# Performance work log

Hardware: AMD Instinct MI355X
Metric: run time of the kernel (lower is better)

Reference implementation:

```python
import jax, jax.numpy as jnp
import numpy as np

B, S, H, D = 2, 2048, 16, 128  # batch, seq, n_head, head_dim; n_embd = H*D
N_EMBD = H * D

def setup_inputs() -> dict:
    key = jax.random.key(0)
    kq, kk, kv = jax.random.split(key, 3)
    q = jax.random.normal(kq, (B, S, H, D), dtype=jnp.float32)
    k = jax.random.normal(kk, (B, S, H, D), dtype=jnp.float32)
    v = jax.random.normal(kv, (B, S, H, D), dtype=jnp.float32)
    return {"q": q, "k": k, "v": v}

def reference(q, k, v):
    # [B,S,H,D] -> [B,H,S,D]
    qh = jnp.transpose(q, (0, 2, 1, 3))
    kh = jnp.transpose(k, (0, 2, 1, 3))
    vh = jnp.transpose(v, (0, 2, 1, 3))
    # scores scaled by head_dim (NOT sqrt), matching the original module
    att = jnp.einsum('bhqd,bhkd->bhqk', qh, kh) / D
    att = jax.nn.softmax(att, axis=-1)
    y = jnp.einsum('bhqk,bhkd->bhqd', att, vh)
    # [B,H,S,D] -> [B,S,H,D] -> [B*S, n_embd]
    y = jnp.transpose(y, (0, 2, 1, 3)).reshape(B * S, N_EMBD)
    return y
```

## Files before the change

kernel.cpp:

```cpp
#include <hip/hip_runtime.h>


#define SEQ   2048
#define NHEAD 16
#define DH    128
#define NB    2
#define BQ    128
#define BK    64
#define NTHR  256
#define KSTR  136
#define VSTR  72
#define NKV   (SEQ / BK)
#define NELEM (NB * SEQ * NHEAD * DH)
#define KTILE (BK * KSTR)
#define VTILE (DH * VSTR)

typedef __attribute__((ext_vector_type(8)))  short bf16x8;
typedef __attribute__((ext_vector_type(16))) float f32x16;
typedef __attribute__((ext_vector_type(4)))  unsigned int u32x4;

__device__ __forceinline__ unsigned short f2bf(float x) {
    unsigned int u = __builtin_bit_cast(unsigned int, x);
    u += 0x7fffu + ((u >> 16) & 1u);
    return (unsigned short)(u >> 16);
}

__device__ __forceinline__ unsigned int bfr(float x) {
    unsigned int u = __builtin_bit_cast(unsigned int, x);
    return (u + 0x8000u) & 0xffff0000u;
}

__device__ __forceinline__ void pl32(unsigned int& a, unsigned int& b) {
    asm("v_permlane32_swap_b32 %0, %1" : "+v"(a), "+v"(b));
}

__global__ __launch_bounds__(256) void cvt_bf16(
    const float* __restrict__ q, const float* __restrict__ k,
    const float* __restrict__ v, unsigned short* __restrict__ dst)
{
    const int y = blockIdx.y;
    const float* s = (y == 0) ? q : (y == 1) ? k : v;
    unsigned short* d = dst + (size_t)y * NELEM;
    const int i = blockIdx.x * 256 + threadIdx.x;
    const float4 x = ((const float4*)s)[i];
    ushort4 o;
    o.x = f2bf(x.x); o.y = f2bf(x.y); o.z = f2bf(x.z); o.w = f2bf(x.w);
    ((ushort4*)d)[i] = o;
}

__global__ __launch_bounds__(NTHR, 2) void attn_fwd(
    const unsigned short* __restrict__ Qb,
    const unsigned short* __restrict__ Kb,
    const unsigned short* __restrict__ Vb,
    float* __restrict__ O)
{
    __shared__ unsigned short Kl[2][KTILE];
    __shared__ unsigned short Vl[2][VTILE];

    const int tid  = threadIdx.x;
    const int wave = tid >> 6;
    const int lane = tid & 63;
    const int hx   = lane >> 5;
    const int l32  = lane & 31;

    const int b  = blockIdx.y >> 4;
    const int h  = blockIdx.y & 15;
    const int q0 = blockIdx.x * BQ;

    const size_t rs = (size_t)NHEAD * DH;
    const unsigned short* qb = Qb + (size_t)b * SEQ * rs + (size_t)h * DH;
    const unsigned short* kb = Kb + (size_t)b * SEQ * rs + (size_t)h * DH;
    const unsigned short* vb = Vb + (size_t)b * SEQ * rs + (size_t)h * DH;

    bf16x8 qf[8];
    {
        const unsigned short* qp = qb + (size_t)(q0 + wave * 32 + l32) * rs + hx * 8;
        #pragma unroll
        for (int c = 0; c < 8; ++c)
            qf[c] = *(const bf16x8*)(qp + c * 16);
    }

    int kgo[4], kls[4];
    #pragma unroll
    for (int p = 0; p < 4; ++p) {
        const int cidx = (wave * 4 + p) * 64 + lane;
        const int key  = cidx >> 4;
        const int cc   = cidx & 15;
        kgo[p] = key * (int)rs + cc * 8;
        kls[p] = key * KSTR + cc * 8;
    }
    const int kp  = tid & 31;
    const int dcv = tid >> 5;

    f32x16 o4[4];
    #pragma unroll
    for (int t = 0; t < 4; ++t)
        #pragma unroll
        for (int r = 0; r < 16; ++r) o4[t][r] = 0.f;
    float lsum = 0.f;
    const float c1 = 1.44269504088896340736f / 128.0f;

    bf16x8 kr[4], vr[4];

    {
        #pragma unroll
        for (int p = 0; p < 4; ++p) kr[p] = *(const bf16x8*)(kb + kgo[p]);
        #pragma unroll
        for (int p = 0; p < 2; ++p) {
            const unsigned short* src = vb + (size_t)(2 * kp) * rs + (dcv + p * 8) * 8;
            vr[p * 2]     = *(const bf16x8*)src;
            vr[p * 2 + 1] = *(const bf16x8*)(src + rs);
        }
        #pragma unroll
        for (int p = 0; p < 4; ++p) *(bf16x8*)&Kl[0][kls[p]] = kr[p];
        unsigned int* vw = (unsigned int*)&Vl[0][0];
        #pragma unroll
        for (int p = 0; p < 2; ++p)
            #pragma unroll
            for (int j = 0; j < 8; ++j) {
                const unsigned int pr = ((unsigned int)(unsigned short)vr[p * 2][j])
                                      | (((unsigned int)(unsigned short)vr[p * 2 + 1][j]) << 16);
                vw[((dcv + p * 8) * 8 + j) * (VSTR / 2) + kp] = pr;
            }
    }
    __syncthreads();

    for (int kv = 0; kv < NKV; ++kv) {
        const int cur = kv & 1;
        const int k0n = ((kv + 1) & (NKV - 1)) * BK;

        #pragma unroll
        for (int p = 0; p < 4; ++p) kr[p] = *(const bf16x8*)(kb + (size_t)k0n * rs + kgo[p]);
        #pragma unroll
        for (int p = 0; p < 2; ++p) {
            const unsigned short* src = vb + (size_t)(k0n + 2 * kp) * rs + (dcv + p * 8) * 8;
            vr[p * 2]     = *(const bf16x8*)src;
            vr[p * 2 + 1] = *(const bf16x8*)(src + rs);
        }

        const unsigned short* Kc = &Kl[cur][0];
        const unsigned short* Vc = &Vl[cur][0];

        #pragma unroll
        for (int kt = 0; kt < 2; ++kt) {
            f32x16 s;
            #pragma unroll
            for (int r = 0; r < 16; ++r) s[r] = 0.f;
            #pragma unroll
            for (int c = 0; c < 8; ++c) {
                bf16x8 kf = *(const bf16x8*)&Kc[(kt * 32 + l32) * KSTR + c * 16 + hx * 8];
                s = __builtin_amdgcn_mfma_f32_32x32x16_bf16(kf, qf[c], s, 0, 0, 0);
            }

            unsigned int w[4][2];
            #pragma unroll
            for (int g = 0; g < 4; ++g) {
                const unsigned int u0 = bfr(__builtin_amdgcn_exp2f(s[g * 4 + 0] * c1));
                const unsigned int u1 = bfr(__builtin_amdgcn_exp2f(s[g * 4 + 1] * c1));
                const unsigned int u2 = bfr(__builtin_amdgcn_exp2f(s[g * 4 + 2] * c1));
                const unsigned int u3 = bfr(__builtin_amdgcn_exp2f(s[g * 4 + 3] * c1));
                lsum += (__builtin_bit_cast(float, u0) + __builtin_bit_cast(float, u1))
                      + (__builtin_bit_cast(float, u2) + __builtin_bit_cast(float, u3));
                w[g][0] = u1 | (u0 >> 16);
                w[g][1] = u3 | (u2 >> 16);
            }

            #pragma unroll
            for (int ks = 0; ks < 2; ++ks) {
                pl32(w[2 * ks][0], w[2 * ks + 1][0]);
                pl32(w[2 * ks][1], w[2 * ks + 1][1]);
            }
            bf16x8 pf[2];
            #pragma unroll
            for (int ks = 0; ks < 2; ++ks) {
                u32x4 t;
                t.x = w[2 * ks][0];
                t.y = w[2 * ks][1];
                t.z = w[2 * ks + 1][0];
                t.w = w[2 * ks + 1][1];
                pf[ks] = __builtin_bit_cast(bf16x8, t);
            }

            #pragma unroll
            for (int ks = 0; ks < 2; ++ks)
                #pragma unroll
                for (int dt = 0; dt < 4; ++dt) {
                    bf16x8 vf = *(const bf16x8*)&Vc[(dt * 32 + l32) * VSTR
                                                    + kt * 32 + ks * 16 + hx * 8];
                    o4[dt] = __builtin_amdgcn_mfma_f32_32x32x16_bf16(pf[ks], vf, o4[dt], 0, 0, 0);
                }
        }

        const int nxt = cur ^ 1;
        #pragma unroll
        for (int p = 0; p < 4; ++p) *(bf16x8*)&Kl[nxt][kls[p]] = kr[p];
        {
            unsigned int* vw = (unsigned int*)&Vl[nxt][0];
            #pragma unroll
            for (int p = 0; p < 2; ++p)
                #pragma unroll
                for (int j = 0; j < 8; ++j) {
                    const unsigned int pr = ((unsigned int)(unsigned short)vr[p * 2][j])
                                          | (((unsigned int)(unsigned short)vr[p * 2 + 1][j]) << 16);
                    vw[((dcv + p * 8) * 8 + j) * (VSTR / 2) + kp] = pr;
                }
        }
        __syncthreads();
    }

    lsum += __shfl_xor(lsum, 32, 64);
    const float inv = 1.0f / lsum;
    float iv[16];
    #pragma unroll
    for (int r = 0; r < 16; ++r)
        iv[r] = __shfl(inv, (r & 3) + 8 * (r >> 2) + 4 * hx, 64);

    #pragma unroll
    for (int dt = 0; dt < 4; ++dt) {
        #pragma unroll
        for (int r = 0; r < 16; ++r) {
            const int ql = (r & 3) + 8 * (r >> 2) + 4 * hx;
            const int qg = q0 + wave * 32 + ql;
            O[(size_t)(b * SEQ + qg) * rs + (size_t)h * DH + dt * 32 + l32] = o4[dt][r] * iv[r];
        }
    }
}

extern "C" void kernel_launch(void* const* d_in, const int* in_sizes, int n_in,
                              void* d_out, int out_size, void* d_ws, size_t ws_size,
                              hipStream_t stream) {
    const float* q = (const float*)d_in[0];
    const float* k = (const float*)d_in[1];
    const float* v = (const float*)d_in[2];
    float* o = (float*)d_out;
    unsigned short* wsb = (unsigned short*)d_ws;

    cvt_bf16<<<dim3(NELEM / 1024, 3), 256, 0, stream>>>(q, k, v, wsb);
    attn_fwd<<<dim3(SEQ / BQ, NB * NHEAD), dim3(NTHR), 0, stream>>>(
        wsb, wsb + NELEM, wsb + 2 * (size_t)NELEM, o);
}
```

Measured before the change: 214.1 us.

## Double query tile and threads per block to share K/V staging

```diff
diff --git a/kernel.cpp b/kernel.cpp
--- a/kernel.cpp
+++ b/kernel.cpp
@@ -5,9 +5,9 @@
 #define NHEAD 16
 #define DH    128
 #define NB    2
-#define BQ    128
+#define BQ    256
 #define BK    64
-#define NTHR  256
+#define NTHR  512
 #define KSTR  136
 #define VSTR  72
 #define NKV   (SEQ / BK)
@@ -80,10 +80,10 @@
             qf[c] = *(const bf16x8*)(qp + c * 16);
     }
 
-    int kgo[4], kls[4];
-    #pragma unroll
-    for (int p = 0; p < 4; ++p) {
-        const int cidx = (wave * 4 + p) * 64 + lane;
+    int kgo[2], kls[2];
+    #pragma unroll
+    for (int p = 0; p < 2; ++p) {
+        const int cidx = p * NTHR + tid;
         const int key  = cidx >> 4;
         const int cc   = cidx & 15;
         kgo[p] = key * (int)rs + cc * 8;
@@ -100,28 +100,25 @@
     float lsum = 0.f;
     const float c1 = 1.44269504088896340736f / 128.0f;
 
-    bf16x8 kr[4], vr[4];
+    bf16x8 kr[2], vr[2];
 
     {
         #pragma unroll
-        for (int p = 0; p < 4; ++p) kr[p] = *(const bf16x8*)(kb + kgo[p]);
-        #pragma unroll
-        for (int p = 0; p < 2; ++p) {
-            const unsigned short* src = vb + (size_t)(2 * kp) * rs + (dcv + p * 8) * 8;
-            vr[p * 2]     = *(const bf16x8*)src;
-            vr[p * 2 + 1] = *(const bf16x8*)(src + rs);
-        }
-        #pragma unroll
-        for (int p = 0; p < 4; ++p) *(bf16x8*)&Kl[0][kls[p]] = kr[p];
+        for (int p = 0; p < 2; ++p) kr[p] = *(const bf16x8*)(kb + kgo[p]);
+        {
+            const unsigned short* src = vb + (size_t)(2 * kp) * rs + dcv * 8;
+            vr[0] = *(const bf16x8*)src;
+            vr[1] = *(const bf16x8*)(src + rs);
+        }
+        #pragma unroll
+        for (int p = 0; p < 2; ++p) *(bf16x8*)&Kl[0][kls[p]] = kr[p];
         unsigned int* vw = (unsigned int*)&Vl[0][0];
         #pragma unroll
-        for (int p = 0; p < 2; ++p)
-            #pragma unroll
-            for (int j = 0; j < 8; ++j) {
-                const unsigned int pr = ((unsigned int)(unsigned short)vr[p * 2][j])
-                                      | (((unsigned int)(unsigned short)vr[p * 2 + 1][j]) << 16);
-                vw[((dcv + p * 8) * 8 + j) * (VSTR / 2) + kp] = pr;
-            }
+        for (int j = 0; j < 8; ++j) {
+            const unsigned int pr = ((unsigned int)(unsigned short)vr[0][j])
+                                  | (((unsigned int)(unsigned short)vr[1][j]) << 16);
+            vw[(dcv * 8 + j) * (VSTR / 2) + kp] = pr;
+        }
     }
     __syncthreads();
 
@@ -130,12 +127,11 @@
         const int k0n = ((kv + 1) & (NKV - 1)) * BK;
 
         #pragma unroll
-        for (int p = 0; p < 4; ++p) kr[p] = *(const bf16x8*)(kb + (size_t)k0n * rs + kgo[p]);
-        #pragma unroll
-        for (int p = 0; p < 2; ++p) {
-            const unsigned short* src = vb + (size_t)(k0n + 2 * kp) * rs + (dcv + p * 8) * 8;
-            vr[p * 2]     = *(const bf16x8*)src;
-            vr[p * 2 + 1] = *(const bf16x8*)(src + rs);
+        for (int p = 0; p < 2; ++p) kr[p] = *(const bf16x8*)(kb + (size_t)k0n * rs + kgo[p]);
+        {
+            const unsigned short* src = vb + (size_t)(k0n + 2 * kp) * rs + dcv * 8;
+            vr[0] = *(const bf16x8*)src;
+            vr[1] = *(const bf16x8*)(src + rs);
         }
 
         const unsigned short* Kc = &Kl[cur][0];
@@ -193,17 +189,15 @@
 
         const int nxt = cur ^ 1;
         #pragma unroll
-        for (int p = 0; p < 4; ++p) *(bf16x8*)&Kl[nxt][kls[p]] = kr[p];
+        for (int p = 0; p < 2; ++p) *(bf16x8*)&Kl[nxt][kls[p]] = kr[p];
         {
             unsigned int* vw = (unsigned int*)&Vl[nxt][0];
             #pragma unroll
-            for (int p = 0; p < 2; ++p)
-                #pragma unroll
-                for (int j = 0; j < 8; ++j) {
-                    const unsigned int pr = ((unsigned int)(unsigned short)vr[p * 2][j])
-                                          | (((unsigned int)(unsigned short)vr[p * 2 + 1][j]) << 16);
-                    vw[((dcv + p * 8) * 8 + j) * (VSTR / 2) + kp] = pr;
-                }
+            for (int j = 0; j < 8; ++j) {
+                const unsigned int pr = ((unsigned int)(unsigned short)vr[0][j])
+                                      | (((unsigned int)(unsigned short)vr[1][j]) << 16);
+                vw[(dcv * 8 + j) * (VSTR / 2) + kp] = pr;
+            }
         }
         __syncthreads();
     }
```

New measurement: 208.9 us. -2.4%, faster.
